# Optimization experiments

Hardware: AMD Instinct MI355X
Metric: run time of the kernel (lower is better)

## Reference

```python
import jax, jax.numpy as jnp
import numpy as np

B, S, NX, H = 8, 1024, 1024, 16
D = NX // H  # head_features = 64
SCALE = True


def setup_inputs() -> dict:
    key = jax.random.key(0)
    k1, k2, k3 = jax.random.split(key, 3)
    x = jax.random.normal(k1, (B, S, NX), dtype=jnp.float32)
    w_attn = jax.random.normal(k2, (NX, 3 * NX), dtype=jnp.float32) * 0.02
    b_attn = jnp.zeros((3 * NX,), dtype=jnp.float32)
    w_proj = jax.random.normal(k3, (NX, NX), dtype=jnp.float32) * 0.02
    b_proj = jnp.zeros((NX,), dtype=jnp.float32)
    return {"x": x, "w_attn": w_attn, "b_attn": b_attn, "w_proj": w_proj, "b_proj": b_proj}


def _split_heads(t):
    # (B, S, NX) -> (B, H, S, D)
    return t.reshape(B, S, H, D).transpose(0, 2, 1, 3)


def reference(x, w_attn, b_attn, w_proj, b_proj):
    # fused QKV projection (Conv1D): addmm over flattened tokens
    qkv = x @ w_attn + b_attn                      # (B, S, 3*NX)
    q, k, v = jnp.split(qkv, 3, axis=-1)
    q = _split_heads(q)                            # (B, H, S, D)
    k = _split_heads(k)
    v = _split_heads(v)

    w = jnp.einsum("bhqd,bhkd->bhqk", q, k)        # full S x S scores
    if SCALE:
        w = w / jnp.sqrt(jnp.asarray(D, w.dtype))
    # causal mask applied exactly as in the source: multiply + big-negative subtract
    b = jnp.tril(jnp.ones((S, S), dtype=w.dtype))[None, None]
    w = w * b - 1e10 * (1.0 - b)
    w = jax.nn.softmax(w, axis=-1)                 # attn_pdrop = 0 (eval)
    a = jnp.einsum("bhqk,bhkd->bhqd", w, v)        # (B, H, S, D)

    # merge heads: (B, H, S, D) -> (B, S, NX)
    a = a.transpose(0, 2, 1, 3).reshape(B, S, NX)
    a = a @ w_proj + b_proj                        # c_proj; resid_pdrop = 0 (eval)
    return a
```

## Files before the change

### kernel.cpp

```cpp
#include <hip/hip_runtime.h>
#include <hip/hip_bf16.h>

#define BB 8
#define SS 1024
#define NXX 1024
#define HH 16
#define DD 64
#define MM (BB * SS)

typedef __attribute__((ext_vector_type(8))) short short8;
typedef __attribute__((ext_vector_type(4))) short short4v;
typedef __attribute__((ext_vector_type(4))) float float4v;

static __device__ inline short bf16bits(float v) {
    __hip_bfloat16 t = __float2bfloat16(v);
    return *reinterpret_cast<short*>(&t);
}

__global__ __launch_bounds__(256) void prep_kernel(
    const float* __restrict__ x, __hip_bfloat16* __restrict__ xb,
    const float* __restrict__ w_attn, __hip_bfloat16* __restrict__ wT_attn,
    const float* __restrict__ w_proj, __hip_bfloat16* __restrict__ wT_proj)
{
    __shared__ __hip_bfloat16 tile[32][33];
    const int blk = blockIdx.x;
    const int tid = threadIdx.x;

    if (blk < 8192) {
        int i = blk * 1024 + tid * 4;
        float4 v = *(const float4*)(x + i);
        xb[i + 0] = __float2bfloat16(v.x);
        xb[i + 1] = __float2bfloat16(v.y);
        xb[i + 2] = __float2bfloat16(v.z);
        xb[i + 3] = __float2bfloat16(v.w);
        return;
    }
    const float* W;
    __hip_bfloat16* Wt;
    int K, N, idx;
    if (blk < 8192 + 3072) { idx = blk - 8192;  W = w_attn; Wt = wT_attn; K = NXX; N = 3 * NXX; }
    else                   { idx = blk - 11264; W = w_proj; Wt = wT_proj; K = NXX; N = NXX; }
    const int k0 = (idx % (K / 32)) * 32;
    const int n0 = (idx / (K / 32)) * 32;
    const int tx = tid % 32;
    const int ty = tid / 32;
#pragma unroll
    for (int p = 0; p < 4; ++p) {
        int k = ty + p * 8;
        tile[k][tx] = __float2bfloat16(W[(size_t)(k0 + k) * N + n0 + tx]);
    }
    __syncthreads();
#pragma unroll
    for (int p = 0; p < 4; ++p) {
        int nn = ty + p * 8;
        Wt[(size_t)(n0 + nn) * K + k0 + tx] = tile[tx][nn];
    }
}

template <int MODE>
__global__ __launch_bounds__(256) void gemm_bf16_mfma(
    const __hip_bfloat16* __restrict__ A,
    const __hip_bfloat16* __restrict__ Bt,
    const float* __restrict__ bias,
    void* __restrict__ Cv,
    __hip_bfloat16* __restrict__ vT,
    int M, int K, int N)
{
    __shared__ __hip_bfloat16 As[128 * 32];
    __shared__ __hip_bfloat16 Bs[128 * 32];

    const int tid  = threadIdx.x;
    const int wave = tid >> 6;
    const int lane = tid & 63;
    const int m0 = blockIdx.x * 128;
    const int n0 = blockIdx.y * 128;
    const int wm = (wave & 1) * 64;
    const int wn = (wave >> 1) * 64;

    float4v acc[4][4];
#pragma unroll
    for (int i = 0; i < 4; ++i)
#pragma unroll
        for (int j = 0; j < 4; ++j) acc[i][j] = (float4v){0.f, 0.f, 0.f, 0.f};

    const int fr = lane & 15;
    const int fk = (lane >> 4) * 8;

    const short* AsS = (const short*)As;
    const short* BsS = (const short*)Bs;

    for (int k0 = 0; k0 < K; k0 += 32) {
#pragma unroll
        for (int j = 0; j < 2; ++j) {
            int c = j * 256 + tid;
            int row = c >> 2;
            int kk = (c & 3) * 8;
            const __hip_bfloat16* ga = A + (size_t)(m0 + row) * K + k0 + kk;
            const __hip_bfloat16* gb = Bt + (size_t)(n0 + row) * K + k0 + kk;
            char* la = (char*)As + j * 4096 + (wave << 10);
            char* lb = (char*)Bs + j * 4096 + (wave << 10);
            __builtin_amdgcn_global_load_lds(
                (const __attribute__((address_space(1))) void*)ga,
                (__attribute__((address_space(3))) void*)la, 16, 0, 0);
            __builtin_amdgcn_global_load_lds(
                (const __attribute__((address_space(1))) void*)gb,
                (__attribute__((address_space(3))) void*)lb, 16, 0, 0);
        }
        __syncthreads();

        short8 a_frag[4], b_frag[4];
#pragma unroll
        for (int i = 0; i < 4; ++i) {
            a_frag[i] = *(const short8*)(AsS + (wm + i * 16 + fr) * 32 + fk);
            b_frag[i] = *(const short8*)(BsS + (wn + i * 16 + fr) * 32 + fk);
        }
#pragma unroll
        for (int i = 0; i < 4; ++i)
#pragma unroll
            for (int j = 0; j < 4; ++j)
                acc[i][j] = __builtin_amdgcn_mfma_f32_16x16x32_bf16(
                    a_frag[i], b_frag[j], acc[i][j], 0, 0, 0);
        __syncthreads();
    }

    const int cr = (lane >> 4) * 4;
    const int cc = lane & 15;

    if (MODE == 1 && n0 >= 2048) {
        const int bb = m0 / SS;
#pragma unroll
        for (int i = 0; i < 4; ++i) {
            int grow = m0 + wm + i * 16 + cr;
            int ssr = grow & (SS - 1);
#pragma unroll
            for (int j = 0; j < 4; ++j) {
                int gcol = n0 + wn + j * 16 + cc;
                float bv = bias[gcol];
                int col = gcol - 2048;
                int hh = col >> 6, dd = col & 63;
                short4v pk;
#pragma unroll
                for (int r = 0; r < 4; ++r) pk[r] = bf16bits(acc[i][j][r] + bv);
                *(short4v*)(vT + (size_t)((bb * HH + hh) * 64 + dd) * SS + ssr) = pk;
            }
        }
    } else {
        const float qs = (MODE == 1 && n0 < 1024) ? 0.125f : 1.0f;
#pragma unroll
        for (int i = 0; i < 4; ++i) {
            int grow = m0 + wm + i * 16 + cr;
#pragma unroll
            for (int j = 0; j < 4; ++j) {
                int gcol = n0 + wn + j * 16 + cc;
                float bv = bias[gcol];
#pragma unroll
                for (int r = 0; r < 4; ++r) {
                    float v = (acc[i][j][r] + bv) * qs;
                    if constexpr (MODE == 1)
                        ((__hip_bfloat16*)Cv)[(size_t)(grow + r) * N + gcol] =
                            __float2bfloat16(v);
                    else
                        ((float*)Cv)[(size_t)(grow + r) * N + gcol] = v;
                }
            }
        }
    }
}

#define PSTR 72

__global__ __launch_bounds__(256) void attn_mfma_kernel(
    const __hip_bfloat16* __restrict__ qkv,
    const __hip_bfloat16* __restrict__ vT,
    __hip_bfloat16* __restrict__ aout)
{
    const int bh = blockIdx.x;
    const int b = bh / HH, h = bh % HH;
    const int q0 = ((int)gridDim.y - 1 - (int)blockIdx.y) * 128;

    __shared__ __hip_bfloat16 Ks[64 * PSTR];
    __shared__ __hip_bfloat16 Vs[64 * PSTR];
    __shared__ __hip_bfloat16 Ps[4][32 * PSTR];

    const int tid  = threadIdx.x;
    const int wave = tid >> 6;
    const int lane = tid & 63;
    const int quad = lane >> 4;
    const int l16  = lane & 15;

    short8 qf[2][2];
#pragma unroll
    for (int t = 0; t < 2; ++t) {
        const __hip_bfloat16* qp = qkv +
            (size_t)(b * SS + q0 + wave * 32 + t * 16 + l16) * 3072 + h * 64 + quad * 8;
        qf[t][0] = *(const short8*)qp;
        qf[t][1] = *(const short8*)(qp + 32);
    }

    float4v o_acc[2][4];
    float l_acc[2][4];
#pragma unroll
    for (int t = 0; t < 2; ++t)
#pragma unroll
        for (int nt = 0; nt < 4; ++nt) o_acc[t][nt] = (float4v){0.f, 0.f, 0.f, 0.f};
#pragma unroll
    for (int t = 0; t < 2; ++t)
#pragma unroll
        for (int r = 0; r < 4; ++r) l_acc[t][r] = 0.f;

    const int sk  = tid & 63;
    const int sdo = (tid >> 6) * 16;
    const int vd  = tid >> 2;
    const int vko = (tid & 3) * 16;
    const int qmin_w = q0 + wave * 32;
    const int nkt = q0 / 64 + 2;

    for (int kt = 0; kt < nkt; ++kt) {
        const int k0 = kt * 64;
        __syncthreads();
        {
            const __hip_bfloat16* kr =
                qkv + (size_t)(b * SS + k0 + sk) * 3072 + 1024 + h * 64 + sdo;
            *(short8*)&Ks[sk * PSTR + sdo]     = *(const short8*)kr;
            *(short8*)&Ks[sk * PSTR + sdo + 8] = *(const short8*)(kr + 8);
            const __hip_bfloat16* vr = vT + (size_t)(bh * 64 + vd) * SS + k0 + vko;
            *(short8*)&Vs[vd * PSTR + vko]     = *(const short8*)vr;
            *(short8*)&Vs[vd * PSTR + vko + 8] = *(const short8*)(vr + 8);
        }
        __syncthreads();
        if (k0 > qmin_w + 31) continue;

        const short* ks = (const short*)Ks;
        float4v sacc[2][4];
#pragma unroll
        for (int t = 0; t < 2; ++t)
#pragma unroll
            for (int nt = 0; nt < 4; ++nt) sacc[t][nt] = (float4v){0.f, 0.f, 0.f, 0.f};
#pragma unroll
        for (int kc = 0; kc < 2; ++kc)
#pragma unroll
            for (int nt = 0; nt < 4; ++nt) {
                short8 kb = *(const short8*)(ks + (nt * 16 + l16) * PSTR + kc * 32 + quad * 8);
                sacc[0][nt] = __builtin_amdgcn_mfma_f32_16x16x32_bf16(qf[0][kc], kb, sacc[0][nt], 0, 0, 0);
                sacc[1][nt] = __builtin_amdgcn_mfma_f32_16x16x32_bf16(qf[1][kc], kb, sacc[1][nt], 0, 0, 0);
            }

        const bool needmask = (k0 + 63 > qmin_w);
        __hip_bfloat16* pw = Ps[wave];
#pragma unroll
        for (int t = 0; t < 2; ++t)
#pragma unroll
            for (int nt = 0; nt < 4; ++nt) {
                int kk = k0 + nt * 16 + l16;
#pragma unroll
                for (int r = 0; r < 4; ++r) {
                    float s = sacc[t][nt][r];
                    if (needmask) {
                        int qq = qmin_w + t * 16 + quad * 4 + r;
                        if (kk > qq) s = -1e10f;
                    }
                    float p = __expf(s);
                    l_acc[t][r] += p;
                    pw[(t * 16 + quad * 4 + r) * PSTR + nt * 16 + l16] =
                        __float2bfloat16(p);
                }
            }

        const short* ps = (const short*)pw;
        const short* vs = (const short*)Vs;
#pragma unroll
        for (int kc = 0; kc < 2; ++kc) {
            short8 pa0 = *(const short8*)(ps + (0 * 16 + l16) * PSTR + kc * 32 + quad * 8);
            short8 pa1 = *(const short8*)(ps + (1 * 16 + l16) * PSTR + kc * 32 + quad * 8);
#pragma unroll
            for (int nt = 0; nt < 4; ++nt) {
                short8 vb = *(const short8*)(vs + (nt * 16 + l16) * PSTR + kc * 32 + quad * 8);
                o_acc[0][nt] = __builtin_amdgcn_mfma_f32_16x16x32_bf16(pa0, vb, o_acc[0][nt], 0, 0, 0);
                o_acc[1][nt] = __builtin_amdgcn_mfma_f32_16x16x32_bf16(pa1, vb, o_acc[1][nt], 0, 0, 0);
            }
        }
    }

#pragma unroll
    for (int t = 0; t < 2; ++t)
#pragma unroll
        for (int r = 0; r < 4; ++r) {
            float l = l_acc[t][r];
            l += __shfl_xor(l, 1);
            l += __shfl_xor(l, 2);
            l += __shfl_xor(l, 4);
            l += __shfl_xor(l, 8);
            float inv = 1.f / l;
            int row = q0 + wave * 32 + t * 16 + quad * 4 + r;
            __hip_bfloat16* op = aout + (size_t)(b * SS + row) * NXX + h * 64 + l16;
#pragma unroll
            for (int nt = 0; nt < 4; ++nt)
                op[nt * 16] = __float2bfloat16(o_acc[t][nt][r] * inv);
        }
}

extern "C" void kernel_launch(void* const* d_in, const int* in_sizes, int n_in,
                              void* d_out, int out_size, void* d_ws, size_t ws_size,
                              hipStream_t stream)
{
    const float* x      = (const float*)d_in[0];
    const float* w_attn = (const float*)d_in[1];
    const float* b_attn = (const float*)d_in[2];
    const float* w_proj = (const float*)d_in[3];
    const float* b_proj = (const float*)d_in[4];
    float* out = (float*)d_out;

    char* ws = (char*)d_ws;
    __hip_bfloat16* qkv     = (__hip_bfloat16*)ws;
    __hip_bfloat16* vT      = (__hip_bfloat16*)(ws + (size_t)48 * 1024 * 1024);
    __hip_bfloat16* xb      = (__hip_bfloat16*)(ws + (size_t)64 * 1024 * 1024);
    __hip_bfloat16* amid    = xb;
    __hip_bfloat16* wT_attn = (__hip_bfloat16*)(ws + (size_t)80 * 1024 * 1024);
    __hip_bfloat16* wT_proj = (__hip_bfloat16*)(ws + (size_t)86 * 1024 * 1024);

    dim3 blk(256);

    prep_kernel<<<dim3(12288), blk, 0, stream>>>(
        x, xb, w_attn, wT_attn, w_proj, wT_proj);

    gemm_bf16_mfma<1><<<dim3(MM / 128, (3 * NXX) / 128), blk, 0, stream>>>(
        xb, wT_attn, b_attn, qkv, vT, MM, NXX, 3 * NXX);

    attn_mfma_kernel<<<dim3(BB * HH, SS / 128), blk, 0, stream>>>(qkv, vT, amid);

    gemm_bf16_mfma<0><<<dim3(MM / 128, NXX / 128), blk, 0, stream>>>(
        amid, wT_proj, b_proj, out, nullptr, MM, NXX, NXX);
}
```

Measured before the change: 247.7 us.

## Replace GEMM with 256x256 tile, double-buffered, swizzled LDS pipeline

Both projection GEMMs move from a 128x128 tile with 256 threads and no overlap to a 256x256 tile with 512 threads, giving each wave 128x64 outputs. LDS is double-buffered so global-to-LDS loads for the next k-step overlap the MFMAs, and explicit waitcnt, barriers and setprio order the phases. An XOR swizzle on the LDS layout is meant to avoid bank conflicts, and the block index is remapped across 8 groups for cache locality. The cost is higher register pressure from 32 accumulators per wave, fewer workgroups, and fragile hand-tuned synchronization.

```diff
diff --git a/kernel.cpp b/kernel.cpp
--- a/kernel.cpp
+++ b/kernel.cpp
@@ -57,8 +57,23 @@
     }
 }
 
+#define STAGE2(SRC, DST, kk)                                                   \
+    {                                                                          \
+        _Pragma("unroll") for (int j_ = 0; j_ < 2; ++j_) {                     \
+            const __hip_bfloat16* s_ = (SRC) + (size_t)(j_ * 128) * K + (kk);  \
+            char* d_ = (char*)(DST) + j_ * 8192 + (wave << 10);                \
+            __builtin_amdgcn_global_load_lds(                                  \
+                (const __attribute__((address_space(1))) void*)s_,             \
+                (__attribute__((address_space(3))) void*)d_, 16, 0, 0);        \
+        }                                                                      \
+    }
+
+#define WAIT_LGKM0_FENCED()                                                    \
+    asm volatile("s_waitcnt lgkmcnt(0)" ::: "memory");                         \
+    __builtin_amdgcn_sched_barrier(0);
+
 template <int MODE>
-__global__ __launch_bounds__(256) void gemm_bf16_mfma(
+__global__ __launch_bounds__(512, 2) void gemm256(
     const __hip_bfloat16* __restrict__ A,
     const __hip_bfloat16* __restrict__ Bt,
     const float* __restrict__ bias,
@@ -66,96 +81,129 @@
     __hip_bfloat16* __restrict__ vT,
     int M, int K, int N)
 {
-    __shared__ __hip_bfloat16 As[128 * 32];
-    __shared__ __hip_bfloat16 Bs[128 * 32];
+    __shared__ __attribute__((aligned(16))) char smem[65536];
 
     const int tid  = threadIdx.x;
     const int wave = tid >> 6;
     const int lane = tid & 63;
-    const int m0 = blockIdx.x * 128;
-    const int n0 = blockIdx.y * 128;
-    const int wm = (wave & 1) * 64;
-    const int wn = (wave >> 1) * 64;
-
-    float4v acc[4][4];
-#pragma unroll
-    for (int i = 0; i < 4; ++i)
+    const int wr = wave >> 2;
+    const int wc = wave & 3;
+
+    const int nwg = (int)gridDim.x;
+    const int cpx = nwg >> 3;
+    const int bid = (int)blockIdx.x;
+    const int swz = (bid & 7) * cpx + (bid >> 3);
+    const int mtiles = M >> 8;
+    const int m0 = (swz % mtiles) << 8;
+    const int n0 = (swz / mtiles) << 8;
+
+    const int NT = K >> 5;
+
+    const int row_s  = tid >> 2;
+    const int srccol = (((tid & 3) ^ ((tid >> 3) & 3)) << 3);
+    const __hip_bfloat16* aSrc = A  + (size_t)(m0 + row_s) * K + srccol;
+    const __hip_bfloat16* bSrc = Bt + (size_t)(n0 + row_s) * K + srccol;
+
+    const int l15 = lane & 15, q4 = lane >> 4;
+    const int skey = (l15 >> 1) & 3;
+    const int sslot = (q4 ^ skey) << 4;
+    const int offA = ((wr << 7) + l15) * 64 + sslot;
+    const int offB = 16384 + ((wc << 6) + l15) * 64 + sslot;
+
+    float4v acc[8][4];
+#pragma unroll
+    for (int i = 0; i < 8; ++i)
 #pragma unroll
         for (int j = 0; j < 4; ++j) acc[i][j] = (float4v){0.f, 0.f, 0.f, 0.f};
 
-    const int fr = lane & 15;
-    const int fk = (lane >> 4) * 8;
-
-    const short* AsS = (const short*)As;
-    const short* BsS = (const short*)Bs;
-
-    for (int k0 = 0; k0 < K; k0 += 32) {
-#pragma unroll
-        for (int j = 0; j < 2; ++j) {
-            int c = j * 256 + tid;
-            int row = c >> 2;
-            int kk = (c & 3) * 8;
-            const __hip_bfloat16* ga = A + (size_t)(m0 + row) * K + k0 + kk;
-            const __hip_bfloat16* gb = Bt + (size_t)(n0 + row) * K + k0 + kk;
-            char* la = (char*)As + j * 4096 + (wave << 10);
-            char* lb = (char*)Bs + j * 4096 + (wave << 10);
-            __builtin_amdgcn_global_load_lds(
-                (const __attribute__((address_space(1))) void*)ga,
-                (__attribute__((address_space(3))) void*)la, 16, 0, 0);
-            __builtin_amdgcn_global_load_lds(
-                (const __attribute__((address_space(1))) void*)gb,
-                (__attribute__((address_space(3))) void*)lb, 16, 0, 0);
-        }
-        __syncthreads();
-
-        short8 a_frag[4], b_frag[4];
-#pragma unroll
-        for (int i = 0; i < 4; ++i) {
-            a_frag[i] = *(const short8*)(AsS + (wm + i * 16 + fr) * 32 + fk);
-            b_frag[i] = *(const short8*)(BsS + (wn + i * 16 + fr) * 32 + fk);
-        }
-#pragma unroll
-        for (int i = 0; i < 4; ++i)
-#pragma unroll
-            for (int j = 0; j < 4; ++j)
-                acc[i][j] = __builtin_amdgcn_mfma_f32_16x16x32_bf16(
-                    a_frag[i], b_frag[j], acc[i][j], 0, 0, 0);
-        __syncthreads();
-    }
-
-    const int cr = (lane >> 4) * 4;
-    const int cc = lane & 15;
+    STAGE2(aSrc, smem, 0);
+    STAGE2(bSrc, smem + 16384, 0);
+    if (NT > 1) {
+        STAGE2(bSrc, smem + 32768 + 16384, 32);
+        asm volatile("s_waitcnt vmcnt(2)" ::: "memory");
+    } else {
+        asm volatile("s_waitcnt vmcnt(0)" ::: "memory");
+    }
+    __builtin_amdgcn_s_barrier();
+
+    for (int t = 0; t < NT; ++t) {
+        char* bufc = (char*)smem + ((t & 1) << 15);
+        char* bufn = (char*)smem + (((t + 1) & 1) << 15);
+        const char* Ab = bufc;
+
+        short8 a[8], b[4];
+
+#pragma unroll
+        for (int mf = 0; mf < 4; ++mf) a[mf] = *(const short8*)(Ab + offA + mf * 1024);
+#pragma unroll
+        for (int nf = 0; nf < 4; ++nf) b[nf] = *(const short8*)(bufc + offB + nf * 1024);
+        if (t + 1 < NT) STAGE2(aSrc, bufn, (t + 1) << 5);
+        __builtin_amdgcn_s_barrier();
+        WAIT_LGKM0_FENCED();
+        __builtin_amdgcn_s_setprio(1);
+#pragma unroll
+        for (int mf = 0; mf < 4; ++mf)
+#pragma unroll
+            for (int nf = 0; nf < 4; ++nf)
+                acc[mf][nf] = __builtin_amdgcn_mfma_f32_16x16x32_bf16(
+                    a[mf], b[nf], acc[mf][nf], 0, 0, 0);
+        __builtin_amdgcn_s_setprio(0);
+        __builtin_amdgcn_s_barrier();
+
+#pragma unroll
+        for (int mf = 0; mf < 4; ++mf) a[mf + 4] = *(const short8*)(Ab + offA + (mf + 4) * 1024);
+        if (t + 2 < NT) {
+            STAGE2(bSrc, bufc + 16384, (t + 2) << 5);
+            asm volatile("s_waitcnt vmcnt(2)" ::: "memory");
+        } else if (t + 1 < NT) {
+            asm volatile("s_waitcnt vmcnt(0)" ::: "memory");
+        }
+        __builtin_amdgcn_s_barrier();
+        WAIT_LGKM0_FENCED();
+        __builtin_amdgcn_s_setprio(1);
+#pragma unroll
+        for (int mf = 0; mf < 4; ++mf)
+#pragma unroll
+            for (int nf = 0; nf < 4; ++nf)
+                acc[mf + 4][nf] = __builtin_amdgcn_mfma_f32_16x16x32_bf16(
+                    a[mf + 4], b[nf], acc[mf + 4][nf], 0, 0, 0);
+        __builtin_amdgcn_s_setprio(0);
+        __builtin_amdgcn_s_barrier();
+    }
+
+    const int cr = q4 * 4;
+    const int cc = l15;
 
     if (MODE == 1 && n0 >= 2048) {
         const int bb = m0 / SS;
 #pragma unroll
-        for (int i = 0; i < 4; ++i) {
-            int grow = m0 + wm + i * 16 + cr;
+        for (int mf = 0; mf < 8; ++mf) {
+            int grow = m0 + (wr << 7) + mf * 16 + cr;
             int ssr = grow & (SS - 1);
 #pragma unroll
-            for (int j = 0; j < 4; ++j) {
-                int gcol = n0 + wn + j * 16 + cc;
+            for (int nf = 0; nf < 4; ++nf) {
+                int gcol = n0 + (wc << 6) + nf * 16 + cc;
                 float bv = bias[gcol];
                 int col = gcol - 2048;
                 int hh = col >> 6, dd = col & 63;
                 short4v pk;
 #pragma unroll
-                for (int r = 0; r < 4; ++r) pk[r] = bf16bits(acc[i][j][r] + bv);
+                for (int r = 0; r < 4; ++r) pk[r] = bf16bits(acc[mf][nf][r] + bv);
                 *(short4v*)(vT + (size_t)((bb * HH + hh) * 64 + dd) * SS + ssr) = pk;
             }
         }
     } else {
         const float qs = (MODE == 1 && n0 < 1024) ? 0.125f : 1.0f;
 #pragma unroll
-        for (int i = 0; i < 4; ++i) {
-            int grow = m0 + wm + i * 16 + cr;
-#pragma unroll
-            for (int j = 0; j < 4; ++j) {
-                int gcol = n0 + wn + j * 16 + cc;
+        for (int mf = 0; mf < 8; ++mf) {
+            int grow = m0 + (wr << 7) + mf * 16 + cr;
+#pragma unroll
+            for (int nf = 0; nf < 4; ++nf) {
+                int gcol = n0 + (wc << 6) + nf * 16 + cc;
                 float bv = bias[gcol];
 #pragma unroll
                 for (int r = 0; r < 4; ++r) {
-                    float v = (acc[i][j][r] + bv) * qs;
+                    float v = (acc[mf][nf][r] + bv) * qs;
                     if constexpr (MODE == 1)
                         ((__hip_bfloat16*)Cv)[(size_t)(grow + r) * N + gcol] =
                             __float2bfloat16(v);
@@ -318,16 +366,14 @@
     __hip_bfloat16* wT_attn = (__hip_bfloat16*)(ws + (size_t)80 * 1024 * 1024);
     __hip_bfloat16* wT_proj = (__hip_bfloat16*)(ws + (size_t)86 * 1024 * 1024);
 
-    dim3 blk(256);
-
-    prep_kernel<<<dim3(12288), blk, 0, stream>>>(
+    prep_kernel<<<dim3(12288), dim3(256), 0, stream>>>(
         x, xb, w_attn, wT_attn, w_proj, wT_proj);
 
-    gemm_bf16_mfma<1><<<dim3(MM / 128, (3 * NXX) / 128), blk, 0, stream>>>(
+    gemm256<1><<<dim3((MM / 256) * ((3 * NXX) / 256)), dim3(512), 0, stream>>>(
         xb, wT_attn, b_attn, qkv, vT, MM, NXX, 3 * NXX);
 
-    attn_mfma_kernel<<<dim3(BB * HH, SS / 128), blk, 0, stream>>>(qkv, vT, amid);
-
-    gemm_bf16_mfma<0><<<dim3(MM / 128, NXX / 128), blk, 0, stream>>>(
+    attn_mfma_kernel<<<dim3(BB * HH, SS / 128), dim3(256), 0, stream>>>(qkv, vT, amid);
+
+    gemm256<0><<<dim3((MM / 256) * (NXX / 256)), dim3(512), 0, stream>>>(
         amid, wT_proj, b_proj, out, nullptr, MM, NXX, NXX);
 }
```

New measurement: 245.5 us. No clear change (-0.9%).
